# Kernel tuning notes

Measured on AMD Instinct MI355X. Metric: run time of the kernel, lower is better.

The kernel has to match this reference:

```python
import jax, jax.numpy as jnp
import numpy as np

NB_HEADS = 12


def setup_inputs() -> dict:
    key = jax.random.key(0)
    ks = jax.random.split(key, 6)
    B, S, D, H = 4, 1024, 768, NB_HEADS
    x = jax.random.normal(ks[0], (B, S, D), dtype=jnp.float32)
    Wqkv = jax.random.normal(ks[1], (D, 3 * D), dtype=jnp.float32) * 0.02
    bqkv = jnp.zeros((3 * D,), dtype=jnp.float32)
    Wl = jax.random.normal(ks[2], (H, H), dtype=jnp.float32) * 0.3
    bl = jnp.zeros((H,), dtype=jnp.float32)
    Ww = jax.random.normal(ks[3], (H, H), dtype=jnp.float32) * 0.3
    bw = jnp.zeros((H,), dtype=jnp.float32)
    Wproj = jax.random.normal(ks[4], (D, D), dtype=jnp.float32) * 0.02
    bproj = jnp.zeros((D,), dtype=jnp.float32)
    return {"x": x, "Wqkv": Wqkv, "bqkv": bqkv, "Wl": Wl, "bl": bl,
            "Ww": Ww, "bw": bw, "Wproj": Wproj, "bproj": bproj}


def reference(x, Wqkv, bqkv, Wl, bl, Ww, bw, Wproj, bproj):
    B, S, D = x.shape
    H = NB_HEADS
    dh = D // H
    scale = dh ** (-0.5)
    # qkv projection: [B,S,3D] -> [3,B,H,S,dh]
    qkv = (x @ Wqkv + bqkv).reshape(B, S, 3, H, dh).transpose(2, 0, 3, 1, 4)
    q, k, v = qkv[0] * scale, qkv[1], qkv[2]
    # raw attention logits [B,H,S,S]
    attn = jnp.einsum('bhqd,bhkd->bhqk', q, k)
    # pre-softmax talking-heads mix across head dim (Dense over heads)
    attn = jnp.einsum('bhqk,hg->bgqk', attn, Wl) + bl[None, :, None, None]
    attn = jax.nn.softmax(attn, axis=-1)
    # post-softmax talking-heads mix
    attn = jnp.einsum('bhqk,hg->bgqk', attn, Ww) + bw[None, :, None, None]
    # attention-weighted values -> [B,S,D]
    out = jnp.einsum('bhqk,bhkd->bqhd', attn, v).reshape(B, S, D)
    return out @ Wproj + bproj
```

## Files before the change

### kernel.cpp

```cpp
#include <hip/hip_runtime.h>
#include <cstdint>

#define BB 4
#define SS 1024
#define DD 768
#define HH 12
#define DH 64

typedef unsigned short u16;
typedef unsigned int   u32;
typedef __attribute__((ext_vector_type(8))) short bf16x8;
typedef __attribute__((ext_vector_type(4))) float f32x4;

__device__ __forceinline__ u16 f2bf(float f) {
    u32 u = __float_as_uint(f);
    u += 0x7fffu + ((u >> 16) & 1u);
    return (u16)(u >> 16);
}
__device__ __forceinline__ float b2f(u32 lo16) {
    return __uint_as_float(lo16 << 16);
}
__device__ __forceinline__ u32 pack2(float a, float b) {
    return (u32)f2bf(a) | ((u32)f2bf(b) << 16);
}

#define ASYNC16(gp, lp) __builtin_amdgcn_global_load_lds( \
    (const __attribute__((address_space(1))) void*)(gp),  \
    (__attribute__((address_space(3))) void*)(lp), 16, 0, 0)

template<int BM_, int BN_, class Epi>
__device__ __forceinline__ void mfma_gemm(
    const u16* __restrict__ A, const u16* __restrict__ B,
    int K, int lda, int ldb, int m0, int n0, const Epi& epi)
{
    constexpr int MI = BM_ / 32;
    constexpr int NJ = BN_ / 32;
    __shared__ u16 Alds[BM_ * 32];
    __shared__ u16 Blds[BN_ * 32];

    const int tid  = threadIdx.x;
    const int wave = tid >> 6;
    const int lane = tid & 63;
    const int wr = wave >> 1, wc = wave & 1;

    const int ar = lane >> 2;
    const int ac = (lane & 3) * 8;

    f32x4 acc[MI][NJ] = {};

    for (int k0 = 0; k0 < K; k0 += 32) {
        __syncthreads();
#pragma unroll
        for (int j = 0; j < BM_ / 64; ++j) {
            const int rb = wave * (BM_ / 4) + j * 16;
            ASYNC16(A + (size_t)(m0 + rb + ar) * lda + k0 + ac, &Alds[rb * 32]);
        }
#pragma unroll
        for (int j = 0; j < BN_ / 64; ++j) {
            const int rb = wave * (BN_ / 4) + j * 16;
            ASYNC16(B + (size_t)(n0 + rb + ar) * ldb + k0 + ac, &Blds[rb * 32]);
        }
        __syncthreads();

        bf16x8 af[MI], bfr[NJ];
#pragma unroll
        for (int mi = 0; mi < MI; ++mi)
            af[mi] = *(const bf16x8*)&Alds[(wr * (BM_ / 2) + mi * 16 + (lane & 15)) * 32 + (lane >> 4) * 8];
#pragma unroll
        for (int nj = 0; nj < NJ; ++nj)
            bfr[nj] = *(const bf16x8*)&Blds[(wc * (BN_ / 2) + nj * 16 + (lane & 15)) * 32 + (lane >> 4) * 8];
#pragma unroll
        for (int mi = 0; mi < MI; ++mi)
#pragma unroll
            for (int nj = 0; nj < NJ; ++nj)
                acc[mi][nj] = __builtin_amdgcn_mfma_f32_16x16x32_bf16(
                    af[mi], bfr[nj], acc[mi][nj], 0, 0, 0);
    }

#pragma unroll
    for (int mi = 0; mi < MI; ++mi)
#pragma unroll
        for (int nj = 0; nj < NJ; ++nj)
#pragma unroll
            for (int r = 0; r < 4; ++r)
                epi(m0 + wr * (BM_ / 2) + mi * 16 + (lane >> 4) * 4 + r,
                    n0 + wc * (BN_ / 2) + nj * 16 + (lane & 15),
                    acc[mi][nj][r]);
}


__global__ __launch_bounds__(256) void qkv_gemm_kernel(
    const u16* __restrict__ xb, const u16* __restrict__ Wt,
    const float* __restrict__ bias,
    u16* __restrict__ qb, u16* __restrict__ kb, u16* __restrict__ vt)
{
    struct Epi {
        const float* bias; u16 *qb, *kb, *vt;
        __device__ void operator()(int m, int n, float v) const {
            const float val = v + bias[n];
            const int c = n / DD;
            const int w = n - c * DD, h = w >> 6, d = w & 63;
            const int b = m >> 10, s = m & 1023;
            if (c == 0)
                qb[(((size_t)(b * HH + h) << 10) + s) * DH + d] = f2bf(val * 0.125f);
            else if (c == 1)
                kb[(((size_t)(b * HH + h) << 10) + s) * DH + d] = f2bf(val);
            else
                vt[((size_t)(b * HH + h) * DH + d) * SS + s] = f2bf(val);
        }
    } epi{bias, qb, kb, vt};
    mfma_gemm<128, 128>(xb, Wt, DD, DD, DD, blockIdx.y * 128, blockIdx.x * 128, epi);
}

__global__ __launch_bounds__(256) void qk_gemm_kernel(
    const u16* __restrict__ qb, const u16* __restrict__ kb,
    u16* __restrict__ attn, int bh0)
{
    const int bhL = blockIdx.z;
    const int bh = bh0 + bhL;
    const u16* A = qb + (size_t)bh * SS * DH;
    const u16* B = kb + (size_t)bh * SS * DH;
    u16* C = attn + (size_t)bhL * SS * SS;
    struct Epi {
        u16* C;
        __device__ void operator()(int m, int n, float v) const {
            C[(size_t)m * SS + n] = f2bf(v);
        }
    } epi{C};
    mfma_gemm<128, 128>(A, B, DH, DH, DH, blockIdx.y * 128, blockIdx.x * 128, epi);
}

__global__ __launch_bounds__(256) void pv_gemm_kernel(
    const u16* __restrict__ attn2, const u16* __restrict__ vt,
    u16* __restrict__ ctx, int bh0)
{
    const int bhL = blockIdx.z;
    const int bh = bh0 + bhL;
    const int b = bh / HH, h = bh % HH;
    const u16* A = attn2 + (size_t)bhL * SS * SS;
    const u16* B = vt + (size_t)bh * DH * SS;
    u16* C = ctx + (size_t)b * SS * DD + h * DH;
    struct Epi {
        u16* C;
        __device__ void operator()(int m, int n, float v) const {
            C[(size_t)m * DD + n] = f2bf(v);
        }
    } epi{C};
    mfma_gemm<128, 64>(A, B, SS, SS, SS, blockIdx.y * 128, 0, epi);
}

__global__ __launch_bounds__(256) void proj_gemm_kernel(
    const u16* __restrict__ ctx, const u16* __restrict__ Wt,
    const float* __restrict__ bias, float* __restrict__ out)
{
    struct Epi {
        float* out; const float* bias;
        __device__ void operator()(int m, int n, float v) const {
            out[(size_t)m * DD + n] = v + bias[n];
        }
    } epi{out, bias};
    mfma_gemm<128, 64>(ctx, Wt, DD, DD, DD, blockIdx.y * 128, blockIdx.x * 64, epi);
}

__global__ __launch_bounds__(256) void mix_softmax_kernel(
    const u16* __restrict__ attn, u16* __restrict__ attn2,
    const float* __restrict__ Wl, const float* __restrict__ bl,
    const float* __restrict__ Ww, const float* __restrict__ bw)
{
    __shared__ float buf[HH][SS];
    __shared__ float invden[HH];

    const int tid  = threadIdx.x;
    const int wave = tid >> 6;
    const int lane = tid & 63;
    const int bL = blockIdx.x >> 10;
    const int qi = blockIdx.x & (SS - 1);
    const size_t gbase = ((size_t)bL * HH * SS + qi) * SS + tid * 4;
    const int kc = tid * 4;

#pragma unroll
    for (int h = 0; h < HH; ++h) {
        const uint2 u = *(const uint2*)&attn[gbase + (size_t)h * SS * SS];
        float4 f;
        f.x = b2f(u.x & 0xffff); f.y = b2f(u.x >> 16);
        f.z = b2f(u.y & 0xffff); f.w = b2f(u.y >> 16);
        *(float4*)&buf[h][kc] = f;
    }

    {
        float4 vin[HH];
#pragma unroll
        for (int h = 0; h < HH; ++h) vin[h] = *(const float4*)&buf[h][kc];
#pragma unroll
        for (int g = 0; g < HH; ++g) {
            float4 s = {bl[g], bl[g], bl[g], bl[g]};
#pragma unroll
            for (int h = 0; h < HH; ++h) {
                const float w = Wl[h * HH + g];
                s.x += vin[h].x * w; s.y += vin[h].y * w;
                s.z += vin[h].z * w; s.w += vin[h].w * w;
            }
            *(float4*)&buf[g][kc] = s;
        }
    }
    __syncthreads();

#pragma unroll
    for (int rep = 0; rep < 3; ++rep) {
        const int g = rep * 4 + wave;
        float4 v[4];
#pragma unroll
        for (int j = 0; j < 4; ++j)
            v[j] = *(const float4*)&buf[g][lane * 4 + j * 256];

        float ps = 0.f;
#pragma unroll
        for (int j = 0; j < 4; ++j) {
            v[j].x = __expf(v[j].x); v[j].y = __expf(v[j].y);
            v[j].z = __expf(v[j].z); v[j].w = __expf(v[j].w);
            ps += (v[j].x + v[j].y) + (v[j].z + v[j].w);
        }
#pragma unroll
        for (int off = 32; off; off >>= 1) ps += __shfl_xor(ps, off);

#pragma unroll
        for (int j = 0; j < 4; ++j)
            *(float4*)&buf[g][lane * 4 + j * 256] = v[j];
        if (lane == 0) invden[g] = 1.0f / ps;
    }
    __syncthreads();

    {
        float4 vin[HH];
#pragma unroll
        for (int h = 0; h < HH; ++h) {
            float4 t = *(const float4*)&buf[h][kc];
            const float inv = invden[h];
            t.x *= inv; t.y *= inv; t.z *= inv; t.w *= inv;
            vin[h] = t;
        }
#pragma unroll
        for (int g = 0; g < HH; ++g) {
            float4 s = {bw[g], bw[g], bw[g], bw[g]};
#pragma unroll
            for (int h = 0; h < HH; ++h) {
                const float w = Ww[h * HH + g];
                s.x += vin[h].x * w; s.y += vin[h].y * w;
                s.z += vin[h].z * w; s.w += vin[h].w * w;
            }
            uint2 p;
            p.x = pack2(s.x, s.y); p.y = pack2(s.z, s.w);
            *(uint2*)&attn2[gbase + (size_t)g * SS * SS] = p;
        }
    }
}


__global__ __launch_bounds__(256) void cvt_bf16_kernel(
    const float* __restrict__ in, u16* __restrict__ out, int n8)
{
    const int i = blockIdx.x * 256 + threadIdx.x;
    if (i >= n8) return;
    const float4 a = ((const float4*)in)[i * 2];
    const float4 b = ((const float4*)in)[i * 2 + 1];
    uint4 p;
    p.x = pack2(a.x, a.y); p.y = pack2(a.z, a.w);
    p.z = pack2(b.x, b.y); p.w = pack2(b.z, b.w);
    ((uint4*)out)[i] = p;
}

__global__ __launch_bounds__(256) void cvt_transpose_kernel(
    const float* __restrict__ in, u16* __restrict__ out, int R, int C)
{
    __shared__ float t[32][33];
    const int c0 = blockIdx.x * 32, r0 = blockIdx.y * 32;
    const int tr = threadIdx.x >> 3;
    const int tc = (threadIdx.x & 7) * 4;
    const float4 v = *(const float4*)&in[(size_t)(r0 + tr) * C + c0 + tc];
    t[tc + 0][tr] = v.x; t[tc + 1][tr] = v.y;
    t[tc + 2][tr] = v.z; t[tc + 3][tr] = v.w;
    __syncthreads();
    uint2 p;
    p.x = pack2(t[tr][tc + 0], t[tr][tc + 1]);
    p.y = pack2(t[tr][tc + 2], t[tr][tc + 3]);
    *(uint2*)&out[(size_t)(c0 + tr) * R + r0 + tc] = p;
}

extern "C" void kernel_launch(void* const* d_in, const int* in_sizes, int n_in,
                              void* d_out, int out_size, void* d_ws, size_t ws_size,
                              hipStream_t stream)
{
    const float* x     = (const float*)d_in[0];
    const float* Wqkv  = (const float*)d_in[1];
    const float* bqkv  = (const float*)d_in[2];
    const float* Wl    = (const float*)d_in[3];
    const float* bl    = (const float*)d_in[4];
    const float* Ww    = (const float*)d_in[5];
    const float* bw    = (const float*)d_in[6];
    const float* Wproj = (const float*)d_in[7];
    const float* bproj = (const float*)d_in[8];
    float* out = (float*)d_out;

    const size_t N_XB  = (size_t)BB * SS * DD;
    const size_t N_QB  = (size_t)BB * HH * SS * DH;
    const size_t N_WT  = (size_t)DD * 3 * DD;
    const size_t N_WP  = (size_t)DD * DD;
    const size_t N_AT1 = (size_t)HH * SS * SS;

    u16* xb  = (u16*)d_ws;
    u16* qb  = xb  + N_XB;
    u16* kb  = qb  + N_QB;
    u16* vt  = kb  + N_QB;
    u16* ctx = vt  + N_QB;
    u16* Wqkv_t = ctx + N_XB;
    u16* Wproj_t = Wqkv_t + N_WT;
    u16* attn = Wproj_t + N_WP;

    const size_t fixed_bytes = (size_t)(N_XB * 2 + N_QB * 3 + N_WT + N_WP) * 2;
    int b_per = BB;
    while (b_per > 1 &&
           fixed_bytes + (size_t)b_per * N_AT1 * 2 * 2 > ws_size)
        b_per >>= 1;
    const int n_iter = BB / b_per;
    u16* attn2 = attn + (size_t)b_per * N_AT1;

    const dim3 blk(256);

    cvt_bf16_kernel<<<dim3((N_XB / 8 + 255) / 256), blk, 0, stream>>>(x, xb, (int)(N_XB / 8));
    cvt_transpose_kernel<<<dim3(3 * DD / 32, DD / 32), blk, 0, stream>>>(Wqkv, Wqkv_t, DD, 3 * DD);
    cvt_transpose_kernel<<<dim3(DD / 32, DD / 32), blk, 0, stream>>>(Wproj, Wproj_t, DD, DD);

    qkv_gemm_kernel<<<dim3(3 * DD / 128, BB * SS / 128), blk, 0, stream>>>(
        xb, Wqkv_t, bqkv, qb, kb, vt);

    for (int it = 0; it < n_iter; ++it) {
        const int bh0 = it * b_per * HH;
        qk_gemm_kernel<<<dim3(SS / 128, SS / 128, b_per * HH), blk, 0, stream>>>(
            qb, kb, attn, bh0);
        mix_softmax_kernel<<<dim3(b_per * SS), blk, 0, stream>>>(
            attn, attn2, Wl, bl, Ww, bw);
        pv_gemm_kernel<<<dim3(1, SS / 128, b_per * HH), blk, 0, stream>>>(
            attn2, vt, ctx, bh0);
    }

    proj_gemm_kernel<<<dim3(DD / 64, BB * SS / 128), blk, 0, stream>>>(
        ctx, Wproj_t, bproj, out);
}
```

Measured before the change: 247.5 us.

## Stage GEMM epilogues through LDS for vectorized stores; transpose V separately

The QKV and QK GEMM kernels are now written inline. Their epilogues stage the accumulator tile in padded LDS and then issue coalesced 16-byte global stores, replacing scattered 2-byte stores. V is written in head-major layout and a new small kernel transposes it into the layout the PV GEMM expects. Before, the QKV epilogue wrote V directly transposed with strided stores. The change costs extra LDS per block (about 34KB for the C tile), which may limit occupancy. It also adds one more launch and an extra V buffer in the workspace.

```diff
diff --git a/kernel.cpp b/kernel.cpp
--- a/kernel.cpp
+++ b/kernel.cpp
@@ -88,47 +88,180 @@
                     acc[mi][nj][r]);
 }
 
+#define CPAD 136
 
 __global__ __launch_bounds__(256) void qkv_gemm_kernel(
     const u16* __restrict__ xb, const u16* __restrict__ Wt,
     const float* __restrict__ bias,
-    u16* __restrict__ qb, u16* __restrict__ kb, u16* __restrict__ vt)
-{
-    struct Epi {
-        const float* bias; u16 *qb, *kb, *vt;
-        __device__ void operator()(int m, int n, float v) const {
-            const float val = v + bias[n];
-            const int c = n / DD;
-            const int w = n - c * DD, h = w >> 6, d = w & 63;
-            const int b = m >> 10, s = m & 1023;
-            if (c == 0)
-                qb[(((size_t)(b * HH + h) << 10) + s) * DH + d] = f2bf(val * 0.125f);
-            else if (c == 1)
-                kb[(((size_t)(b * HH + h) << 10) + s) * DH + d] = f2bf(val);
-            else
-                vt[((size_t)(b * HH + h) * DH + d) * SS + s] = f2bf(val);
-        }
-    } epi{bias, qb, kb, vt};
-    mfma_gemm<128, 128>(xb, Wt, DD, DD, DD, blockIdx.y * 128, blockIdx.x * 128, epi);
+    u16* __restrict__ qb, u16* __restrict__ kb, u16* __restrict__ vb)
+{
+    __shared__ u16 Alds[128 * 32];
+    __shared__ u16 Blds[128 * 32];
+    __shared__ u16 Clds[128 * CPAD];
+
+    const int tid  = threadIdx.x;
+    const int wave = tid >> 6;
+    const int lane = tid & 63;
+    const int wr = wave >> 1, wc = wave & 1;
+    const int ar = lane >> 2;
+    const int ac = (lane & 3) * 8;
+    const int m0 = blockIdx.y * 128, n0 = blockIdx.x * 128;
+
+    f32x4 acc[4][4] = {};
+
+    for (int k0 = 0; k0 < DD; k0 += 32) {
+        __syncthreads();
+#pragma unroll
+        for (int j = 0; j < 2; ++j) {
+            const int rb = wave * 32 + j * 16;
+            ASYNC16(xb + (size_t)(m0 + rb + ar) * DD + k0 + ac, &Alds[rb * 32]);
+            ASYNC16(Wt + (size_t)(n0 + rb + ar) * DD + k0 + ac, &Blds[rb * 32]);
+        }
+        __syncthreads();
+
+        bf16x8 af[4], bfr[4];
+#pragma unroll
+        for (int mi = 0; mi < 4; ++mi)
+            af[mi] = *(const bf16x8*)&Alds[(wr * 64 + mi * 16 + (lane & 15)) * 32 + (lane >> 4) * 8];
+#pragma unroll
+        for (int nj = 0; nj < 4; ++nj)
+            bfr[nj] = *(const bf16x8*)&Blds[(wc * 64 + nj * 16 + (lane & 15)) * 32 + (lane >> 4) * 8];
+#pragma unroll
+        for (int mi = 0; mi < 4; ++mi)
+#pragma unroll
+            for (int nj = 0; nj < 4; ++nj)
+                acc[mi][nj] = __builtin_amdgcn_mfma_f32_16x16x32_bf16(
+                    af[mi], bfr[nj], acc[mi][nj], 0, 0, 0);
+    }
+
+    const int c  = n0 / DD;
+    const int w0 = n0 - c * DD;
+    const int hA = w0 >> 6;
+    const float qs = (c == 0) ? 0.125f : 1.0f;
+#pragma unroll
+    for (int mi = 0; mi < 4; ++mi)
+#pragma unroll
+        for (int nj = 0; nj < 4; ++nj)
+#pragma unroll
+            for (int r = 0; r < 4; ++r) {
+                const int row = wr * 64 + mi * 16 + (lane >> 4) * 4 + r;
+                const int col = wc * 64 + nj * 16 + (lane & 15);
+                Clds[row * CPAD + col] = f2bf((acc[mi][nj][r] + bias[n0 + col]) * qs);
+            }
+    __syncthreads();
+
+    u16* const dst = (c == 0) ? qb : (c == 1) ? kb : vb;
+    const int b = m0 >> 10;
+#pragma unroll
+    for (int j = 0; j < 8; ++j) {
+        const int idx = j * 256 + tid;
+        const int row = idx >> 4, u4 = idx & 15;
+        const int half = u4 >> 3, d8 = u4 & 7;
+        const int h = hA + half;
+        const int s = (m0 + row) & 1023;
+        const uint4 v = *(const uint4*)&Clds[row * CPAD + half * 64 + d8 * 8];
+        *(uint4*)&dst[(((size_t)(b * HH + h) << 10) + s) * DH + d8 * 8] = v;
+    }
+}
+
+__global__ __launch_bounds__(256) void vtrans_kernel(
+    const u16* __restrict__ vb, u16* __restrict__ vt)
+{
+    __shared__ u16 t[64 * 72];
+    const int tid = threadIdx.x;
+    const int bh = blockIdx.y;
+    const int s0 = blockIdx.x * 64;
+    const u16* src = vb + ((size_t)bh << 16) + (size_t)s0 * DH;
+
+#pragma unroll
+    for (int j = 0; j < 2; ++j) {
+        const int idx = j * 256 + tid;
+        const int row = idx >> 3, u4 = idx & 7;
+        *(uint4*)&t[row * 72 + u4 * 8] = *(const uint4*)&src[row * DH + u4 * 8];
+    }
+    __syncthreads();
+
+#pragma unroll
+    for (int j = 0; j < 2; ++j) {
+        const int idx = j * 256 + tid;
+        const int d = idx >> 3, u4 = idx & 7;
+        u16 tmp[8];
+#pragma unroll
+        for (int i = 0; i < 8; ++i) tmp[i] = t[(u4 * 8 + i) * 72 + d];
+        *(uint4*)&vt[((size_t)bh * DH + d) * SS + s0 + u4 * 8] = *(const uint4*)tmp;
+    }
 }
 
 __global__ __launch_bounds__(256) void qk_gemm_kernel(
     const u16* __restrict__ qb, const u16* __restrict__ kb,
     u16* __restrict__ attn, int bh0)
 {
+    __shared__ u16 Alds[128 * 32];
+    __shared__ u16 Blds[128 * 32];
+    __shared__ u16 Clds[128 * CPAD];
+
+    const int tid  = threadIdx.x;
+    const int wave = tid >> 6;
+    const int lane = tid & 63;
+    const int wr = wave >> 1, wc = wave & 1;
+    const int ar = lane >> 2;
+    const int ac = (lane & 3) * 8;
+    const int m0 = blockIdx.y * 128, n0 = blockIdx.x * 128;
+
     const int bhL = blockIdx.z;
-    const int bh = bh0 + bhL;
-    const u16* A = qb + (size_t)bh * SS * DH;
-    const u16* B = kb + (size_t)bh * SS * DH;
+    const u16* A = qb + (size_t)(bh0 + bhL) * SS * DH;
+    const u16* B = kb + (size_t)(bh0 + bhL) * SS * DH;
     u16* C = attn + (size_t)bhL * SS * SS;
-    struct Epi {
-        u16* C;
-        __device__ void operator()(int m, int n, float v) const {
-            C[(size_t)m * SS + n] = f2bf(v);
-        }
-    } epi{C};
-    mfma_gemm<128, 128>(A, B, DH, DH, DH, blockIdx.y * 128, blockIdx.x * 128, epi);
-}
+
+    f32x4 acc[4][4] = {};
+
+#pragma unroll
+    for (int k0 = 0; k0 < DH; k0 += 32) {
+        __syncthreads();
+#pragma unroll
+        for (int j = 0; j < 2; ++j) {
+            const int rb = wave * 32 + j * 16;
+            ASYNC16(A + (size_t)(m0 + rb + ar) * DH + k0 + ac, &Alds[rb * 32]);
+            ASYNC16(B + (size_t)(n0 + rb + ar) * DH + k0 + ac, &Blds[rb * 32]);
+        }
+        __syncthreads();
+
+        bf16x8 af[4], bfr[4];
+#pragma unroll
+        for (int mi = 0; mi < 4; ++mi)
+            af[mi] = *(const bf16x8*)&Alds[(wr * 64 + mi * 16 + (lane & 15)) * 32 + (lane >> 4) * 8];
+#pragma unroll
+        for (int nj = 0; nj < 4; ++nj)
+            bfr[nj] = *(const bf16x8*)&Blds[(wc * 64 + nj * 16 + (lane & 15)) * 32 + (lane >> 4) * 8];
+#pragma unroll
+        for (int mi = 0; mi < 4; ++mi)
+#pragma unroll
+            for (int nj = 0; nj < 4; ++nj)
+                acc[mi][nj] = __builtin_amdgcn_mfma_f32_16x16x32_bf16(
+                    af[mi], bfr[nj], acc[mi][nj], 0, 0, 0);
+    }
+
+#pragma unroll
+    for (int mi = 0; mi < 4; ++mi)
+#pragma unroll
+        for (int nj = 0; nj < 4; ++nj)
+#pragma unroll
+            for (int r = 0; r < 4; ++r) {
+                const int row = wr * 64 + mi * 16 + (lane >> 4) * 4 + r;
+                const int col = wc * 64 + nj * 16 + (lane & 15);
+                Clds[row * CPAD + col] = f2bf(acc[mi][nj][r]);
+            }
+    __syncthreads();
+
+#pragma unroll
+    for (int j = 0; j < 8; ++j) {
+        const int idx = j * 256 + tid;
+        const int row = idx >> 4, u4 = idx & 15;
+        *(uint4*)&C[(size_t)(m0 + row) * SS + n0 + u4 * 8] =
+            *(const uint4*)&Clds[row * CPAD + u4 * 8];
+    }
+}
+
 
 __global__ __launch_bounds__(256) void pv_gemm_kernel(
     const u16* __restrict__ attn2, const u16* __restrict__ vt,
@@ -310,13 +443,14 @@
     u16* xb  = (u16*)d_ws;
     u16* qb  = xb  + N_XB;
     u16* kb  = qb  + N_QB;
-    u16* vt  = kb  + N_QB;
+    u16* vb  = kb  + N_QB;
+    u16* vt  = vb  + N_QB;
     u16* ctx = vt  + N_QB;
     u16* Wqkv_t = ctx + N_XB;
     u16* Wproj_t = Wqkv_t + N_WT;
     u16* attn = Wproj_t + N_WP;
 
-    const size_t fixed_bytes = (size_t)(N_XB * 2 + N_QB * 3 + N_WT + N_WP) * 2;
+    const size_t fixed_bytes = (size_t)(N_XB * 2 + N_QB * 4 + N_WT + N_WP) * 2;
     int b_per = BB;
     while (b_per > 1 &&
            fixed_bytes + (size_t)b_per * N_AT1 * 2 * 2 > ws_size)
@@ -331,7 +465,9 @@
     cvt_transpose_kernel<<<dim3(DD / 32, DD / 32), blk, 0, stream>>>(Wproj, Wproj_t, DD, DD);
 
     qkv_gemm_kernel<<<dim3(3 * DD / 128, BB * SS / 128), blk, 0, stream>>>(
-        xb, Wqkv_t, bqkv, qb, kb, vt);
+        xb, Wqkv_t, bqkv, qb, kb, vb);
+
+    vtrans_kernel<<<dim3(SS / 64, BB * HH), blk, 0, stream>>>(vb, vt);
 
     for (int it = 0; it < n_iter; ++it) {
         const int bh0 = it * b_per * HH;
```

Result: faster. 239.5 us (-3.2%).
